# Kernel tuning notes

Hardware: AMD Instinct MI355X
Metric: run time of the kernel (lower is better)

## Reference

```python
import jax, jax.numpy as jnp
import numpy as np

TAU = 0.1
K = 60.0
CHUNK = 64
B = 1024


def setup_inputs() -> dict:
    key = jax.random.key(0)
    k1, k2, k3, k4 = jax.random.split(key, 4)
    s_v = jax.random.normal(k1, (B, B), jnp.float32)
    s_l = jax.random.normal(k2, (B, B), jnp.float32)
    # class-label based positive/negative masks (typical metric-learning batch)
    labels = jax.random.randint(k3, (B,), 0, B // 8)
    pos_mask = labels[:, None] == labels[None, :]
    neg_mask = ~pos_mask
    w_v = jax.random.uniform(k4, (B, B), jnp.float32)
    w_l = 1.0 - w_v
    return dict(s_v=s_v, s_l=s_l, pos_mask=pos_mask, neg_mask=neg_mask, w_v=w_v, w_l=w_l)


def _soft_ranks(sim, pos_f, neg_f, tau=TAU, chunk=CHUNK):
    """Row-chunked differentiable soft ranks. sim/pos_f/neg_f: [B, B] float."""
    b = sim.shape[0]
    nc = b // chunk  # B divisible by chunk

    def body(args):
        cs, cp, cn = args                                   # [chunk, B] each
        # sig[c, k, j] = sigmoid((s_ck - s_cj) / tau)
        sig = jax.nn.sigmoid((cs[:, :, None] - cs[:, None, :]) / tau)
        rank_pos = 1.0 + jnp.einsum('ckj,ck->cj', sig, cn)  # count negatives above
        rank_neg = 1.0 + jnp.einsum('ckj,ck->cj', sig, cp)  # count positives above
        return rank_pos * cp + rank_neg * cn

    args = (sim.reshape(nc, chunk, b), pos_f.reshape(nc, chunk, b), neg_f.reshape(nc, chunk, b))
    return jax.lax.map(jax.checkpoint(body), args).reshape(b, b)


def reference(s_v, s_l, pos_mask, neg_mask, w_v, w_l):
    pos_f = pos_mask.astype(s_v.dtype)
    neg_f = neg_mask.astype(s_v.dtype)
    rank_v = _soft_ranks(s_v, pos_f, neg_f)
    rank_l = _soft_ranks(s_l, pos_f, neg_f)
    S_hat = (K + 1.0) * (w_v / (K + rank_v) + w_l / (K + rank_l))
    return S_hat
```

## Files before the change

kernel.cpp:

```cpp
#include <hip/hip_runtime.h>


#define NB 1024
#define CEXP 14.426950408889634f
#define SCL  0.000030517578125f
#define NBUK 86
#define BUK0 4.3f
#define BUKW 10.0f
#define DBUK 3
#define CHSZ 128
#define NJOB 32
#define MAXPOS 64

__device__ __forceinline__ float fma_sat(float a, float b, float c) {
    float d;
    asm("v_fma_f32 %0, %1, %2, %3 clamp" : "=v"(d) : "v"(a), "v"(b), "v"(c));
    return d;
}

__device__ __forceinline__ float nrcp(float d) {
    float r = __uint_as_float(0x7EF311C3u - __float_as_uint(d));
    r = r * fmaf(-d, r, 2.0f);
    return r;
}

#define TREE(Es, ra, rb, A)                                      \
    {                                                            \
        const float y1 = fma_sat((Es), (ra).x, SCL);             \
        const float y2 = fma_sat((Es), (ra).y, SCL);             \
        const float y3 = fma_sat((Es), (ra).z, SCL);             \
        const float y4 = fma_sat((Es), (ra).w, SCL);             \
        const float y5 = fma_sat((Es), (rb).x, SCL);             \
        const float y6 = fma_sat((Es), (rb).y, SCL);             \
        const float y7 = fma_sat((Es), (rb).z, SCL);             \
        const float y8 = fma_sat((Es), (rb).w, SCL);             \
        const float p12 = y1 * y2, p34 = y3 * y4;                \
        const float p56 = y5 * y6, p78 = y7 * y8;                \
        const float s12 = y1 + y2, s34 = y3 + y4;                \
        const float s56 = y5 + y6, s78 = y7 + y8;                \
        const float q1 = p12 * p34, q2 = p56 * p78;              \
        const float n1 = fmaf(s12, p34, s34 * p12);              \
        const float n2 = fmaf(s56, p78, s78 * p56);              \
        const float num = fmaf(n1, q2, n2 * q1);                 \
        const float den = q1 * q2;                               \
        (A) = fmaf(num, nrcp(den), (A));                         \
    }

__global__ __launch_bounds__(512) void drank_kernel(
    const float* __restrict__ s_v, const float* __restrict__ s_l,
    const unsigned char* __restrict__ pos_m,
    const unsigned char* __restrict__ neg_m,
    const float* __restrict__ w_v, const float* __restrict__ w_l,
    float* __restrict__ out)
{
    __shared__ float  listRv[NB], listRl[NB];
    __shared__ int    listJv[NB], listJl[NB];
    __shared__ float  sAv1[NB], sAl1[NB];
    __shared__ float  sAv2[NB], sAl2[NB];
    __shared__ int    offv[NBUK + 1], offl[NBUK + 1];
    __shared__ float2 posR[MAXPOS];
    __shared__ int    npos_s, jobCtr;

    int* curv = (int*)sAv1;
    int* curl = (int*)sAl1;

    const int c = blockIdx.x;
    const int t = threadIdx.x;
    const long row = (long)c * NB;

    if (t < NBUK) { curv[t] = 0; curl[t] = 0; }
    if (t == 0) { npos_s = 0; jobCtr = 0; }
    __syncthreads();

    const unsigned int W =
        ((const unsigned int*)pos_m)[0] ^ ((const unsigned int*)neg_m)[0];
    const int mode = (W == 0x01010101u) ? 0 : ((W == 0x3f800000u) ? 2 : 1);

    const int j0 = t * 2;
    const float2 sjv = *(const float2*)(s_v + row + j0);
    const float2 sjl = *(const float2*)(s_l + row + j0);
    const float svu[2] = {sjv.x, sjv.y};
    const float slu[2] = {sjl.x, sjl.y};

    float Rv[2], Rl[2], Ev[2], El[2];
    int ibv[2], ibl[2];
    #pragma unroll
    for (int u = 0; u < 2; ++u) {
        Rv[u] = __builtin_amdgcn_exp2f(-svu[u] * CEXP);
        Rl[u] = __builtin_amdgcn_exp2f(-slu[u] * CEXP);
        Ev[u] = __builtin_amdgcn_exp2f(svu[u] * CEXP);
        El[u] = __builtin_amdgcn_exp2f(slu[u] * CEXP);
        ibv[u] = max(0, min(NBUK - 1, (int)((svu[u] + BUK0) * BUKW)));
        ibl[u] = max(0, min(NBUK - 1, (int)((slu[u] + BUK0) * BUKW)));
        atomicAdd(&curv[ibv[u]], 1);
        atomicAdd(&curl[ibl[u]], 1);
    }

    bool pj[2];
    if (mode == 0) {
        const unsigned short b = ((const unsigned short*)pos_m)[(row >> 1) + t];
        pj[0] = (b & 0x00ffu) != 0; pj[1] = (b & 0xff00u) != 0;
    } else if (mode == 2) {
        const float2 p = *(const float2*)((const float*)pos_m + row + j0);
        pj[0] = p.x != 0.f; pj[1] = p.y != 0.f;
    } else {
        const int2 p = *(const int2*)((const int*)pos_m + row + j0);
        pj[0] = p.x != 0; pj[1] = p.y != 0;
    }
    #pragma unroll
    for (int u = 0; u < 2; ++u) {
        if (pj[u]) {
            const int idx = atomicAdd(&npos_s, 1);
            if (idx < MAXPOS) posR[idx] = make_float2(Rv[u], Rl[u]);
        }
    }
    __syncthreads();

    if (t == 0) {
        int a = 0;
        for (int b = 0; b < NBUK; ++b) { offv[b] = a; a += curv[b]; }
        offv[NBUK] = a;
    }
    if (t == 64) {
        int a = 0;
        for (int b = 0; b < NBUK; ++b) { offl[b] = a; a += curl[b]; }
        offl[NBUK] = a;
    }
    __syncthreads();
    if (t < NBUK) { curv[t] = offv[t]; curl[t] = offl[t]; }
    __syncthreads();

    #pragma unroll
    for (int u = 0; u < 2; ++u) {
        const int pv = atomicAdd(&curv[ibv[u]], 1);
        listRv[pv] = Rv[u];
        listJv[pv] = (j0 + u) | (ibv[u] << 16);
        const int pl = atomicAdd(&curl[ibl[u]], 1);
        listRl[pl] = Rl[u];
        listJl[pl] = (j0 + u) | (ibl[u] << 16);
    }
    __syncthreads();

    static const unsigned char CORD[8] = {3, 4, 2, 5, 1, 6, 0, 7};
    const int lane = t & 63;

    for (;;) {
        int jid0 = 0;
        if (lane == 0) jid0 = atomicAdd(&jobCtr, 1);
        const int jid = __builtin_amdgcn_readfirstlane(jid0);
        if (jid >= NJOB) break;
        const int ch = CORD[jid >> 2];
        const int m  = (jid >> 1) & 1;
        const int h  = jid & 1;

        const float*  LR  = m ? listRl : listRv;
        const int*    LJ  = m ? listJl : listJv;
        const int*    off = m ? offl : offv;
        float*        SA  = h ? (m ? sAl2 : sAv2) : (m ? sAl1 : sAv1);
        const float4* L4  = (const float4*)LR;

        const int p0 = ch * CHSZ + 2 * lane;
        const float2 R2 = *(const float2*)(LR + p0);
        const int2   jj = *(const int2*)(LJ + p0);
        const float EsX = SCL * __builtin_amdgcn_rcpf(R2.x);
        const float EsY = SCL * __builtin_amdgcn_rcpf(R2.y);

        const int bs = LJ[ch * CHSZ] >> 16;
        const int be = LJ[ch * CHSZ + CHSZ - 1] >> 16;
        const int lo0 = off[max(0, bs - DBUK)] & ~7;
        const int hi0 = (off[min(NBUK - 1, be + DBUK) + 1] + 7) & ~7;
        const int mid = ((lo0 + hi0) >> 1) & ~7;
        const int lo = h ? mid : lo0;
        const int hi = h ? hi0 : mid;

        float a0 = 0.f, a1 = 0.f;
        #pragma unroll 2
        for (int p = lo; p < hi; p += 8) {
            const float4 ra = L4[p >> 2];
            const float4 rb = L4[(p >> 2) + 1];
            TREE(EsX, ra, rb, a0);
            TREE(EsY, ra, rb, a1);
        }
        const float cnt = h ? (float)(NB - hi0) : 0.0f;
        SA[jj.x & 0xFFFF] = fmaf(a0, SCL, cnt);
        SA[jj.y & 0xFFFF] = fmaf(a1, SCL, cnt);
    }

    float sPv[2] = {0.f, 0.f};
    float sPl[2] = {0.f, 0.f};
    const int np = min(npos_s, MAXPOS);
    for (int i = 0; i < np; ++i) {
        const float2 rp = posR[i];
        #pragma unroll
        for (int u = 0; u < 2; ++u) {
            sPv[u] += __builtin_amdgcn_rcpf(fmaf(Ev[u], rp.x, 1.0f));
            sPl[u] += __builtin_amdgcn_rcpf(fmaf(El[u], rp.y, 1.0f));
        }
    }
    __syncthreads();

    const float2 av1 = *(const float2*)(sAv1 + j0);
    const float2 av2 = *(const float2*)(sAv2 + j0);
    const float2 al1 = *(const float2*)(sAl1 + j0);
    const float2 al2 = *(const float2*)(sAl2 + j0);
    const float sAvu[2] = {av1.x + av2.x, av1.y + av2.y};
    const float sAlu[2] = {al1.x + al2.x, al1.y + al2.y};
    const float2 wv = *(const float2*)(w_v + row + j0);
    const float2 wl = *(const float2*)(w_l + row + j0);
    const float wva[2] = {wv.x, wv.y};
    const float wla[2] = {wl.x, wl.y};
    float o[2];
    #pragma unroll
    for (int u = 0; u < 2; ++u) {
        const float rv = pj[u] ? (1.0f + sAvu[u] - sPv[u]) : (1.0f + sPv[u]);
        const float rl = pj[u] ? (1.0f + sAlu[u] - sPl[u]) : (1.0f + sPl[u]);
        o[u] = 61.0f * (wva[u] / (60.0f + rv) + wla[u] / (60.0f + rl));
    }
    float2 o2;
    o2.x = o[0]; o2.y = o[1];
    *(float2*)(out + row + j0) = o2;
}

extern "C" void kernel_launch(void* const* d_in, const int* in_sizes, int n_in,
                              void* d_out, int out_size, void* d_ws, size_t ws_size,
                              hipStream_t stream) {
    const float* s_v = (const float*)d_in[0];
    const float* s_l = (const float*)d_in[1];
    const unsigned char* pos_m = (const unsigned char*)d_in[2];
    const unsigned char* neg_m = (const unsigned char*)d_in[3];
    const float* w_v = (const float*)d_in[4];
    const float* w_l = (const float*)d_in[5];
    float* out = (float*)d_out;

    drank_kernel<<<dim3(NB), dim3(512), 0, stream>>>(s_v, s_l, pos_m, neg_m, w_v, w_l, out);
}
```

Baseline: 128.2 us.

## Narrow bucket window and add first-order tail corrections via prefix sums

Reduces the bucket neighbour window (DBUK 3→2) so each job scans fewer list entries in the pairwise sigmoid loop. To compensate for the truncated window, it builds per-8-element prefix sums of R and 1/R in shared memory and adds first-order correction terms (1 - E*R tail and R*E head) instead of treating out-of-window sigmoids as exactly 0 or 1. This trades some inner-loop work for an extra reduction phase with serial scans and a couple more barriers, and changes numerical accuracy slightly.

```diff
diff --git a/kernel.cpp b/kernel.cpp
--- a/kernel.cpp
+++ b/kernel.cpp
@@ -7,7 +7,7 @@
 #define NBUK 86
 #define BUK0 4.3f
 #define BUKW 10.0f
-#define DBUK 3
+#define DBUK 2
 #define CHSZ 128
 #define NJOB 32
 #define MAXPOS 64
@@ -58,6 +58,8 @@
     __shared__ float  sAv1[NB], sAl1[NB];
     __shared__ float  sAv2[NB], sAl2[NB];
     __shared__ int    offv[NBUK + 1], offl[NBUK + 1];
+    __shared__ float  SRv[129], SEv[129];
+    __shared__ float  SRl[129], SEl[129];
     __shared__ float2 posR[MAXPOS];
     __shared__ int    npos_s, jobCtr;
 
@@ -141,6 +143,32 @@
     }
     __syncthreads();
 
+    if (t < 256) {
+        const int m = t >> 7, o = t & 127;
+        const float4* L4 = (const float4*)(m ? listRl : listRv);
+        const float4 a = L4[2 * o], b = L4[2 * o + 1];
+        const float sR = ((a.x + a.y) + (a.z + a.w)) + ((b.x + b.y) + (b.z + b.w));
+        const float sE =
+            ((__builtin_amdgcn_rcpf(a.x) + __builtin_amdgcn_rcpf(a.y)) +
+             (__builtin_amdgcn_rcpf(a.z) + __builtin_amdgcn_rcpf(a.w))) +
+            ((__builtin_amdgcn_rcpf(b.x) + __builtin_amdgcn_rcpf(b.y)) +
+             (__builtin_amdgcn_rcpf(b.z) + __builtin_amdgcn_rcpf(b.w)));
+        (m ? SRl : SRv)[o] = sR;
+        (m ? SEl : SEv)[o] = sE;
+    }
+    __syncthreads();
+    if (t == 0)   { float a = 0; SRv[128] = 0;
+                    for (int o = 127; o >= 0; --o) { a += SRv[o]; SRv[o] = a; } }
+    if (t == 64)  { float a = 0;
+                    for (int o = 0; o < 128; ++o) { const float x = SEv[o]; SEv[o] = a; a += x; }
+                    SEv[128] = a; }
+    if (t == 128) { float a = 0; SRl[128] = 0;
+                    for (int o = 127; o >= 0; --o) { a += SRl[o]; SRl[o] = a; } }
+    if (t == 192) { float a = 0;
+                    for (int o = 0; o < 128; ++o) { const float x = SEl[o]; SEl[o] = a; a += x; }
+                    SEl[128] = a; }
+    __syncthreads();
+
     static const unsigned char CORD[8] = {3, 4, 2, 5, 1, 6, 0, 7};
     const int lane = t & 63;
 
@@ -157,13 +185,17 @@
         const int*    LJ  = m ? listJl : listJv;
         const int*    off = m ? offl : offv;
         float*        SA  = h ? (m ? sAl2 : sAv2) : (m ? sAl1 : sAv1);
+        const float*  SR  = m ? SRl : SRv;
+        const float*  SE  = m ? SEl : SEv;
         const float4* L4  = (const float4*)LR;
 
         const int p0 = ch * CHSZ + 2 * lane;
         const float2 R2 = *(const float2*)(LR + p0);
         const int2   jj = *(const int2*)(LJ + p0);
-        const float EsX = SCL * __builtin_amdgcn_rcpf(R2.x);
-        const float EsY = SCL * __builtin_amdgcn_rcpf(R2.y);
+        const float Ex = __builtin_amdgcn_rcpf(R2.x);
+        const float Ey = __builtin_amdgcn_rcpf(R2.y);
+        const float EsX = SCL * Ex;
+        const float EsY = SCL * Ey;
 
         const int bs = LJ[ch * CHSZ] >> 16;
         const int be = LJ[ch * CHSZ + CHSZ - 1] >> 16;
@@ -181,9 +213,18 @@
             TREE(EsX, ra, rb, a0);
             TREE(EsY, ra, rb, a1);
         }
-        const float cnt = h ? (float)(NB - hi0) : 0.0f;
-        SA[jj.x & 0xFFFF] = fmaf(a0, SCL, cnt);
-        SA[jj.y & 0xFFFF] = fmaf(a1, SCL, cnt);
+        float cx, cy;
+        if (h) {
+            const float sr = SR[hi0 >> 3];
+            cx = fmaf(-Ex, sr, (float)(NB - hi0));
+            cy = fmaf(-Ey, sr, (float)(NB - hi0));
+        } else {
+            const float se = SE[lo0 >> 3];
+            cx = R2.x * se;
+            cy = R2.y * se;
+        }
+        SA[jj.x & 0xFFFF] = fmaf(a0, SCL, cx);
+        SA[jj.y & 0xFFFF] = fmaf(a1, SCL, cy);
     }
 
     float sPv[2] = {0.f, 0.f};
```

Measured after the change: 124.9 us. 1.03x faster.

## Add second-order tail corrections and finer buckets to narrow the sigmoid window

Applied to the files above, without the earlier changes.

Raises the bucket count and shrinks the neighbour window around each chunk, so the exact sigmoid loop covers fewer elements. The sigmoid mass left outside the window is approximated with a first- plus second-order expansion, using per-8-block prefix sums of R, 1/R and their squares built with wavefront scans. The serial bucket-offset scan is also replaced with a shuffle-based parallel prefix. This adds a prefix pass and series error in the truncated tails in exchange for less inner-loop work.

```diff
diff --git a/kernel.cpp b/kernel.cpp
--- a/kernel.cpp
+++ b/kernel.cpp
@@ -4,13 +4,14 @@
 #define NB 1024
 #define CEXP 14.426950408889634f
 #define SCL  0.000030517578125f
-#define NBUK 86
+#define NBUK 128
 #define BUK0 4.3f
-#define BUKW 10.0f
-#define DBUK 3
+#define BUKW 14.883720930f
+#define DBUK 2
 #define CHSZ 128
 #define NJOB 32
 #define MAXPOS 64
+#define ECLMP 1e17f
 
 __device__ __forceinline__ float fma_sat(float a, float b, float c) {
     float d;
@@ -58,6 +59,10 @@
     __shared__ float  sAv1[NB], sAl1[NB];
     __shared__ float  sAv2[NB], sAl2[NB];
     __shared__ int    offv[NBUK + 1], offl[NBUK + 1];
+    __shared__ float  SRv[129], SEv[129];
+    __shared__ float  SR2v[129], SE2v[129];
+    __shared__ float  SRl[129], SEl[129];
+    __shared__ float  SR2l[129], SE2l[129];
     __shared__ float2 posR[MAXPOS];
     __shared__ int    npos_s, jobCtr;
 
@@ -116,18 +121,22 @@
     }
     __syncthreads();
 
-    if (t == 0) {
-        int a = 0;
-        for (int b = 0; b < NBUK; ++b) { offv[b] = a; a += curv[b]; }
-        offv[NBUK] = a;
-    }
-    if (t == 64) {
-        int a = 0;
-        for (int b = 0; b < NBUK; ++b) { offl[b] = a; a += curl[b]; }
-        offl[NBUK] = a;
-    }
-    __syncthreads();
-    if (t < NBUK) { curv[t] = offv[t]; curl[t] = offl[t]; }
+    if (t < 128) {
+        const int m = t >> 6, l = t & 63;
+        int* cnt = m ? curl : curv;
+        int* off = m ? offl : offv;
+        const int c0 = cnt[2 * l], c1 = cnt[2 * l + 1];
+        int s = c0 + c1;
+        #pragma unroll
+        for (int d = 1; d < 64; d <<= 1) {
+            const int y = __shfl_up(s, d, 64);
+            if (l >= d) s += y;
+        }
+        const int excl = s - c0 - c1;
+        off[2 * l] = excl;     off[2 * l + 1] = excl + c0;
+        cnt[2 * l] = excl;     cnt[2 * l + 1] = excl + c0;
+        if (l == 63) off[NBUK] = s;
+    }
     __syncthreads();
 
     #pragma unroll
@@ -141,6 +150,53 @@
     }
     __syncthreads();
 
+    {
+        const int wid = t >> 6, l = t & 63;
+        const int m   = (wid >> 1) & 1;
+        const int fE  = wid & 1;
+        const int sq  = wid >> 2;
+        const float4* L4 = (const float4*)(m ? listRl : listRv);
+        float* arr;
+        switch (wid) {
+            case 0: arr = SRv;  break;  case 1: arr = SEv;  break;
+            case 2: arr = SRl;  break;  case 3: arr = SEl;  break;
+            case 4: arr = SR2v; break;  case 5: arr = SE2v; break;
+            case 6: arr = SR2l; break;  default: arr = SE2l; break;
+        }
+        const int o0 = fE ? (2 * l) : (127 - 2 * l);
+        const int o1 = fE ? (2 * l + 1) : (126 - 2 * l);
+        float s01[2];
+        #pragma unroll
+        for (int q = 0; q < 2; ++q) {
+            const int o = q ? o1 : o0;
+            const float4 a = L4[2 * o], b = L4[2 * o + 1];
+            float x[8] = {a.x, a.y, a.z, a.w, b.x, b.y, b.z, b.w};
+            float acc = 0.f;
+            #pragma unroll
+            for (int i = 0; i < 8; ++i) {
+                float v = fE ? __builtin_amdgcn_rcpf(x[i]) : x[i];
+                v = fminf(v, ECLMP);
+                acc += sq ? v * v : v;
+            }
+            s01[q] = acc;
+        }
+        float s = s01[0] + s01[1];
+        #pragma unroll
+        for (int d = 1; d < 64; d <<= 1) {
+            const float y = __shfl_up(s, d, 64);
+            if (l >= d) s += y;
+        }
+        if (fE) {
+            const float excl = s - s01[0] - s01[1];
+            arr[o0] = excl;  arr[o1] = excl + s01[0];
+            if (l == 63) arr[128] = s;
+        } else {
+            arr[o1] = s;  arr[o0] = s - s01[1];
+            if (l == 0) arr[128] = 0.f;
+        }
+    }
+    __syncthreads();
+
     static const unsigned char CORD[8] = {3, 4, 2, 5, 1, 6, 0, 7};
     const int lane = t & 63;
 
@@ -157,13 +213,19 @@
         const int*    LJ  = m ? listJl : listJv;
         const int*    off = m ? offl : offv;
         float*        SA  = h ? (m ? sAl2 : sAv2) : (m ? sAl1 : sAv1);
+        const float*  SR  = m ? SRl : SRv;
+        const float*  SE  = m ? SEl : SEv;
+        const float*  SR2 = m ? SR2l : SR2v;
+        const float*  SE2 = m ? SE2l : SE2v;
         const float4* L4  = (const float4*)LR;
 
         const int p0 = ch * CHSZ + 2 * lane;
         const float2 R2 = *(const float2*)(LR + p0);
         const int2   jj = *(const int2*)(LJ + p0);
-        const float EsX = SCL * __builtin_amdgcn_rcpf(R2.x);
-        const float EsY = SCL * __builtin_amdgcn_rcpf(R2.y);
+        const float Ex = __builtin_amdgcn_rcpf(R2.x);
+        const float Ey = __builtin_amdgcn_rcpf(R2.y);
+        const float EsX = SCL * Ex;
+        const float EsY = SCL * Ey;
 
         const int bs = LJ[ch * CHSZ] >> 16;
         const int be = LJ[ch * CHSZ + CHSZ - 1] >> 16;
@@ -181,9 +243,20 @@
             TREE(EsX, ra, rb, a0);
             TREE(EsY, ra, rb, a1);
         }
-        const float cnt = h ? (float)(NB - hi0) : 0.0f;
-        SA[jj.x & 0xFFFF] = fmaf(a0, SCL, cnt);
-        SA[jj.y & 0xFFFF] = fmaf(a1, SCL, cnt);
+        float cx, cy;
+        if (h) {
+            const float sr = SR[hi0 >> 3], sr2 = SR2[hi0 >> 3];
+            const float Exc = fminf(Ex, ECLMP), Eyc = fminf(Ey, ECLMP);
+            cx = (float)(NB - hi0) - Exc * sr + (Exc * Exc) * sr2;
+            cy = (float)(NB - hi0) - Eyc * sr + (Eyc * Eyc) * sr2;
+        } else {
+            const float se = SE[lo0 >> 3], se2 = SE2[lo0 >> 3];
+            const float Rxc = fminf(R2.x, ECLMP), Ryc = fminf(R2.y, ECLMP);
+            cx = Rxc * se - (Rxc * Rxc) * se2;
+            cy = Ryc * se - (Ryc * Ryc) * se2;
+        }
+        SA[jj.x & 0xFFFF] = fmaf(a0, SCL, cx);
+        SA[jj.y & 0xFFFF] = fmaf(a1, SCL, cy);
     }
 
     float sPv[2] = {0.f, 0.f};
```

After: 117.2 us. 1.09x faster.
